# Kernel optimization log

Hardware: AMD Instinct MI355X
Metric: run time of the kernel (lower is better)

Reference implementation:

```python
import jax, jax.numpy as jnp
import numpy as np

N_NODES = 50000
N_EDGES = 800000
IN_FEATS = 256
N_HIDDEN = 256
N_CLASSES = 47


def _glorot(key, shape):
    fan_in, fan_out = shape
    lim = (6.0 / (fan_in + fan_out)) ** 0.5
    return jax.random.uniform(key, shape, jnp.float32, -lim, lim)


def setup_inputs() -> dict:
    key = jax.random.key(0)
    ks = jax.random.split(key, 12)
    x = jax.random.normal(ks[0], (N_NODES, IN_FEATS), jnp.float32)
    src = jax.random.randint(ks[1], (N_EDGES,), 0, N_NODES, jnp.int64)
    dst = jax.random.randint(ks[2], (N_EDGES,), 0, N_NODES, jnp.int64)
    dims = [(IN_FEATS, N_HIDDEN), (N_HIDDEN, N_HIDDEN), (N_HIDDEN, N_CLASSES)]
    inp = {"x": x, "src": src, "dst": dst}
    for i, (di, do) in enumerate(dims):
        inp[f"Wself{i}"] = _glorot(ks[3 + 3 * i], (di, do))
        inp[f"Wneigh{i}"] = _glorot(ks[4 + 3 * i], (di, do))
        inp[f"b{i}"] = jnp.zeros((do,), jnp.float32)
    return inp


def _sage_layer(h, src, dst, Ws, Wn, b):
    # DGL mean SAGEConv: fc_self(h) + fc_neigh(mean over in-neighbors) + bias
    msum = jax.ops.segment_sum(h[src], dst, num_segments=N_NODES)      # [N, d]
    deg = jax.ops.segment_sum(jnp.ones((src.shape[0],), h.dtype), dst,
                              num_segments=N_NODES)                     # [N]
    hmean = msum / jnp.maximum(deg, 1.0)[:, None]
    return h @ Ws + hmean @ Wn + b


def reference(x, src, dst, Wself0, Wneigh0, b0, Wself1, Wneigh1, b1,
              Wself2, Wneigh2, b2):
    h = _sage_layer(x, src, dst, Wself0, Wneigh0, b0)
    h = jax.nn.selu(h)
    h = _sage_layer(h, src, dst, Wself1, Wneigh1, b1)
    h = jax.nn.selu(h)
    h = _sage_layer(h, src, dst, Wself2, Wneigh2, b2)
    return jax.nn.softmax(h, axis=1)
```

## Files before the change

### kernel.cpp

```cpp
#include <hip/hip_runtime.h>
#include <math.h>

#define FEATS 256
#define KTOT  512
#define MS    264
#define SA    40

typedef __attribute__((ext_vector_type(8))) __bf16 bf16x8;
typedef __attribute__((ext_vector_type(4))) float f32x4;

#define ASYNC16(G, L) __builtin_amdgcn_global_load_lds( \
    (const __attribute__((address_space(1))) unsigned int*)(G), \
    (__attribute__((address_space(3))) unsigned int*)(L), 16, 0, 0)

__device__ __forceinline__ float bf2f(unsigned short u) {
    union { unsigned int i; float f; } v; v.i = ((unsigned int)u) << 16; return v.f;
}
__device__ __forceinline__ unsigned short f2bf(float f) {
    unsigned int u = __float_as_uint(f);
    unsigned int r = (u + 0x7FFFu + ((u >> 16) & 1u)) >> 16;
    return (unsigned short)r;
}
__device__ __forceinline__ unsigned short rdw(const void* W, size_t i, bool f32m) {
    return f32m ? f2bf(((const float*)W)[i]) : ((const unsigned short*)W)[i];
}

__global__ void k_detect(const int* __restrict__ srcRaw, const unsigned short* __restrict__ xr,
                         int nE, int* __restrict__ flag) {
    __shared__ int any, cnt;
    if (threadIdx.x == 0) { any = 0; cnt = 0; }
    __syncthreads();
    int lim = nE < 1024 ? nE : 1024;
    for (int i = threadIdx.x; i < lim; i += 256)
        if (srcRaw[2 * i + 1] != 0) atomicAdd(&any, 1);
    int loc = 0;
    for (int i = threadIdx.x; i < 1024; i += 256) {
        unsigned e = (xr[2 * i] >> 7) & 255u;
        if (e >= 90u && e <= 140u) loc++;
    }
    atomicAdd(&cnt, loc);
    __syncthreads();
    if (threadIdx.x == 0) {
        flag[0] = (any == 0) ? 1 : 0;
        flag[1] = (cnt > 512) ? 1 : 0;
    }
}

__global__ void k_count(const int* __restrict__ dstRaw, int* __restrict__ deg, int nE,
                        int nNodes, const int* __restrict__ flag) {
    int e = blockIdx.x * 256 + threadIdx.x;
    if (e >= nE) return;
    int f = flag[0];
    int d = dstRaw[f ? (2 * e) : e];
    if ((unsigned)d >= (unsigned)nNodes) d = 0;
    atomicAdd(&deg[d], 1);
}

__global__ __launch_bounds__(256) void k_bsum(const int* __restrict__ deg, int* __restrict__ bsum,
                                              int n) {
    __shared__ int buf[256];
    const int t = threadIdx.x;
    int i = blockIdx.x * 256 + t;
    buf[t] = (i < n) ? deg[i] : 0;
    __syncthreads();
    for (int s = 128; s > 0; s >>= 1) {
        if (t < s) buf[t] += buf[t + s];
        __syncthreads();
    }
    if (t == 0) bsum[blockIdx.x] = buf[0];
}

__global__ __launch_bounds__(256) void k_scanb(int* __restrict__ bsum, int nB) {
    __shared__ int buf[256];
    __shared__ int carry;
    const int t = threadIdx.x;
    if (t == 0) carry = 0;
    __syncthreads();
    for (int base = 0; base < nB; base += 256) {
        int i = base + t;
        int v = (i < nB) ? bsum[i] : 0;
        buf[t] = v;
        __syncthreads();
        for (int s = 1; s < 256; s <<= 1) {
            int tv = (t >= s) ? buf[t - s] : 0;
            __syncthreads();
            buf[t] += tv;
            __syncthreads();
        }
        int exc = buf[t] - v;
        int c = carry;
        if (i < nB) bsum[i] = c + exc;
        int tot = buf[255];
        __syncthreads();
        if (t == 0) carry = c + tot;
        __syncthreads();
    }
}

__global__ __launch_bounds__(256) void k_offs(const int* __restrict__ deg,
                                              const int* __restrict__ bsum,
                                              int* __restrict__ off, int* __restrict__ cursor,
                                              int n) {
    __shared__ int buf[256];
    const int t = threadIdx.x, b = blockIdx.x;
    int i = b * 256 + t;
    int v = (i < n) ? deg[i] : 0;
    buf[t] = v;
// ... 22 lines not shown
    int pos = atomicAdd(&cursor[d], 1);
    csr[pos] = s;
}

__global__ __launch_bounds__(256) void k_buildAll(
        const void* __restrict__ Ws0, const void* __restrict__ Wn0,
        const void* __restrict__ Ws1, const void* __restrict__ Wn1,
        const void* __restrict__ Ws2, const void* __restrict__ Wn2,
        unsigned short* __restrict__ Wt0, unsigned short* __restrict__ Wt1,
        unsigned short* __restrict__ Wt2s, unsigned short* __restrict__ Wt2n,
        int C, const int* __restrict__ flag) {
    const bool f32m = (flag[1] == 0);
    int idx = blockIdx.x * 256 + threadIdx.x;
    if (idx < 262144) {
        const bool one = idx >= 131072;
        int j = one ? idx - 131072 : idx;
        int n = j >> 9, k = j & 511;
        const void* Ws = one ? Ws1 : Ws0;
        const void* Wn = one ? Wn1 : Wn0;
        unsigned short v = (k < 256) ? rdw(Ws, (size_t)k * 256 + n, f32m)
                                     : rdw(Wn, (size_t)(k - 256) * 256 + n, f32m);
        (one ? Wt1 : Wt0)[j] = v;
    } else if (idx < 294912) {
        const bool nw = idx >= 278528;
        int j = nw ? idx - 278528 : idx - 262144;
        int n = j >> 8, k = j & 255;
        unsigned short v = 0;
        if (n < C) v = rdw(nw ? Wn2 : Ws2, (size_t)k * C + n, f32m);
        (nw ? Wt2n : Wt2s)[j] = v;
    }
}

__global__ __launch_bounds__(256) void k_aggr(
        const void* __restrict__ h, const int* __restrict__ off,
        const int* __restrict__ csr, unsigned short* __restrict__ hmean,
        int M, const int* __restrict__ flag, int maybeF32) {
    const bool f32m = maybeF32 && (flag[1] == 0);
    const int lane = threadIdx.x & 63;
    const int wid = (blockIdx.x * 256 + threadIdx.x) >> 6;
    const int nw = (gridDim.x * 256) >> 6;
    if (f32m) {
        for (int r = wid; r < M; r += nw) {
            const int e0 = off[r], e1 = off[r + 1];
            float a0 = 0.f, a1 = 0.f, a2 = 0.f, a3 = 0.f;
            for (int base = e0; base < e1; base += 64) {
                int cnt = e1 - base; if (cnt > 64) cnt = 64;
                int sidx = (lane < cnt) ? csr[base + lane] : 0;
                #pragma unroll 8
                for (int d = 0; d < cnt; d++) {
                    int s = __shfl(sidx, d);
                    float4 hv = reinterpret_cast<const float4*>(
                        (const float*)h + (size_t)s * FEATS)[lane];
                    a0 += hv.x; a1 += hv.y; a2 += hv.z; a3 += hv.w;
                }
            }
            float rc = 1.0f / fmaxf((float)(e1 - e0), 1.0f);
            ushort4 o;
            o.x = f2bf(a0 * rc); o.y = f2bf(a1 * rc); o.z = f2bf(a2 * rc); o.w = f2bf(a3 * rc);
            *reinterpret_cast<ushort4*>(&hmean[(size_t)r * FEATS + lane * 4]) = o;
        }
    } else {
        for (int r = wid; r < M; r += nw) {
            const int e0 = off[r], e1 = off[r + 1];
            float a0 = 0.f, a1 = 0.f, a2 = 0.f, a3 = 0.f;
            for (int base = e0; base < e1; base += 64) {
                int cnt = e1 - base; if (cnt > 64) cnt = 64;
                int sidx = (lane < cnt) ? csr[base + lane] : 0;
                #pragma unroll 8
                for (int d = 0; d < cnt; d++) {
                    int s = __shfl(sidx, d);
                    ushort4 hv = reinterpret_cast<const ushort4*>(
                        (const unsigned short*)h + (size_t)s * FEATS)[lane];
                    a0 += bf2f(hv.x); a1 += bf2f(hv.y); a2 += bf2f(hv.z); a3 += bf2f(hv.w);
                }
            }
            float rc = 1.0f / fmaxf((float)(e1 - e0), 1.0f);
            ushort4 o;
            o.x = f2bf(a0 * rc); o.y = f2bf(a1 * rc); o.z = f2bf(a2 * rc); o.w = f2bf(a3 * rc);
            *reinterpret_cast<ushort4*>(&hmean[(size_t)r * FEATS + lane * 4]) = o;
        }
    }
}

__global__ __launch_bounds__(256) void k_aggrP(
        const unsigned short* __restrict__ P, const int* __restrict__ off,
        const int* __restrict__ csr, unsigned short* __restrict__ A, int M) {
    const int lane = threadIdx.x & 63;
    const int wid = (blockIdx.x * 256 + threadIdx.x) >> 6;
    const int nw = (gridDim.x * 256) >> 6;
    const int g = lane >> 5, li = lane & 31;
    for (int r = wid; r < M; r += nw) {
        const int e0 = off[r], e1 = off[r + 1];
        float a0 = 0.f, a1 = 0.f;
        #pragma unroll 4
        for (int base = e0; base < e1; base += 2) {
            int e = base + g;
            if (e < e1) {
                int s = csr[e];
                ushort2 hv = *reinterpret_cast<const ushort2*>(
                    P + (size_t)s * 64 + li * 2);
                a0 += bf2f(hv.x); a1 += bf2f(hv.y);
            }
        }
        a0 += __shfl_xor(a0, 32); a1 += __shfl_xor(a1, 32);
        if (g == 0) {
            float rc = 1.0f / fmaxf((float)(e1 - e0), 1.0f);
            unsigned int packed = (unsigned int)f2bf(a0 * rc) |
                                  ((unsigned int)f2bf(a1 * rc) << 16);
            *reinterpret_cast<unsigned int*>(&A[(size_t)r * 64 + li * 2]) = packed;
        }
    }
}

__global__ __launch_bounds__(256) void k_gemm(
        const void* __restrict__ h, const unsigned short* __restrict__ hmean,
        const unsigned short* __restrict__ Wt, const void* __restrict__ bias,
        void* __restrict__ out, int M, const int* __restrict__ flag, int maybeF32) {
    const bool inF32 = (flag[1] == 0);
    const bool hF32 = maybeF32 && inF32;
    __shared__ __align__(16) unsigned short As[64 * 64];
    __shared__ __align__(16) unsigned short Bs[128 * 64];

    const int rb = (int)blockIdx.x >> 1;
    const int chalf = (int)blockIdx.x & 1;
    const int m0 = rb * 64;
    const int col0 = chalf * 128;
    const int tid = threadIdx.x;
    const int lane = tid & 63, w = tid >> 6;
    const int nh = lane & 15, q = lane >> 4;

    f32x4 acc[8];
    #pragma unroll
    for (int ci = 0; ci < 8; ci++) acc[ci] = (f32x4){0.f, 0.f, 0.f, 0.f};

    for (int kb = 0; kb < KTOT; kb += 64) {
        #pragma unroll
        for (int j = 0; j < 2; j++) {
            int t2 = tid + j * 256;
            int row = t2 >> 3, c = t2 & 7;
            int gr = m0 + row; if (gr > M - 1) gr = M - 1;
            int cs = c ^ (row & 7);
            if (kb < 256) {
                if (hF32) {
                    const float* p = (const float*)h + (size_t)gr * FEATS + kb + cs * 8;
                    float4 a = *reinterpret_cast<const float4*>(p);
                    float4 b = *reinterpret_cast<const float4*>(p + 4);
                    unsigned short* d = &As[t2 * 8];
                    d[0]=f2bf(a.x); d[1]=f2bf(a.y); d[2]=f2bf(a.z); d[3]=f2bf(a.w);
                    d[4]=f2bf(b.x); d[5]=f2bf(b.y); d[6]=f2bf(b.z); d[7]=f2bf(b.w);
                } else {
                    ASYNC16((const unsigned short*)h + (size_t)gr * FEATS + kb + cs * 8,
                            &As[t2 * 8]);
                }
            } else {
                ASYNC16(hmean + (size_t)gr * FEATS + (kb - 256) + cs * 8, &As[t2 * 8]);
            }
        }
        #pragma unroll
        for (int j = 0; j < 4; j++) {
            int t2 = tid + j * 256;
            int n = t2 >> 3, c = t2 & 7;
            int cs = c ^ (n & 7);
            ASYNC16(Wt + (size_t)(col0 + n) * KTOT + kb + cs * 8, &Bs[t2 * 8]);
        }
        __syncthreads();

        #pragma unroll
        for (int s = 0; s < 2; s++) {
            const int arow = w * 16 + nh;
            const int qa = ((s * 4 + q) ^ (arow & 7));
            bf16x8 afr = *reinterpret_cast<const bf16x8*>(&As[arow * 64 + qa * 8]);
            #pragma unroll
            for (int ci = 0; ci < 8; ci++) {
                int n = ci * 16 + nh;
                int qb = ((s * 4 + q) ^ (n & 7));
                bf16x8 bfr = *reinterpret_cast<const bf16x8*>(&Bs[n * 64 + qb * 8]);
                acc[ci] = __builtin_amdgcn_mfma_f32_16x16x32_bf16(afr, bfr, acc[ci], 0, 0, 0);
            }
        }
        __syncthreads();
    }

    const int rbase = m0 + w * 16 + q * 4;
    const float sc = 1.0507009873554805f, al = 1.6732632423543772f;
    #pragma unroll
    for (int ci = 0; ci < 8; ci++) {
        int col = col0 + ci * 16 + nh;
        float b = inF32 ? ((const float*)bias)[col] : bf2f(((const unsigned short*)bias)[col]);
        #pragma unroll
        for (int rg = 0; rg < 4; rg++) {
            int r = rbase + rg;
            if (r < M) {
                float v = acc[ci][rg] + b;
                v = (v > 0.f) ? sc * v : sc * al * expm1f(v);
                ((unsigned short*)out)[(size_t)r * FEATS + col] = f2bf(v);
            }
        }
    }
}

__global__ __launch_bounds__(256) void k_gemm256d(
        const unsigned short* __restrict__ h, const unsigned short* __restrict__ Wt2s,
        const unsigned short* __restrict__ Wt2n, float* __restrict__ S2,
        unsigned short* __restrict__ P2, int M) {
    __shared__ __align__(16) unsigned short As[64 * SA];
    __shared__ __align__(16) unsigned short Bs[128 * SA];

    const int m0 = blockIdx.x * 64;
    const int tid = threadIdx.x;
    const int lane = tid & 63, w = tid >> 6;
    const int nh = lane & 15, q = lane >> 4;

    f32x4 acc[8];
    #pragma unroll
    for (int ci = 0; ci < 8; ci++) acc[ci] = (f32x4){0.f, 0.f, 0.f, 0.f};

    for (int kb = 0; kb < 256; kb += 32) {
        {
            int row = tid >> 2, seg = tid & 3;
            int gr = m0 + row; if (gr > M - 1) gr = M - 1;
            *reinterpret_cast<float4*>(&As[row * SA + seg * 8]) =
                *reinterpret_cast<const float4*>(h + (size_t)gr * FEATS + kb + seg * 8);
        }
        for (int u = tid; u < 128 * 4; u += 256) {
            int nn = u >> 2, seg = u & 3;
            const unsigned short* src = (nn < 64)
                ? Wt2s + (size_t)nn * 256 : Wt2n + (size_t)(nn - 64) * 256;
            *reinterpret_cast<float4*>(&Bs[nn * SA + seg * 8]) =
                *reinterpret_cast<const float4*>(src + kb + seg * 8);
        }
        __syncthreads();
        bf16x8 afr = *reinterpret_cast<const bf16x8*>(&As[(w * 16 + nh) * SA + q * 8]);
        #pragma unroll
        for (int ci = 0; ci < 8; ci++) {
            bf16x8 bfr = *reinterpret_cast<const bf16x8*>(&Bs[(ci * 16 + nh) * SA + q * 8]);
            acc[ci] = __builtin_amdgcn_mfma_f32_16x16x32_bf16(afr, bfr, acc[ci], 0, 0, 0);
        }
        __syncthreads();
    }

    const int rbase = m0 + w * 16 + q * 4;
    #pragma unroll
    for (int ci = 0; ci < 4; ci++) {
        int col = ci * 16 + nh;
        #pragma unroll
        for (int rg = 0; rg < 4; rg++) {
            int r = rbase + rg;
            if (r < M) S2[(size_t)r * 64 + col] = acc[ci][rg];
        }
    }
    #pragma unroll
    for (int ci = 4; ci < 8; ci++) {
        int col = (ci - 4) * 16 + nh;
        #pragma unroll
        for (int rg = 0; rg < 4; rg++) {
            int r = rbase + rg;
            if (r < M) P2[(size_t)r * 64 + col] = f2bf(acc[ci][rg]);
        }
    }
}

__global__ __launch_bounds__(256) void k_smax(
        const float* __restrict__ S2, const unsigned short* __restrict__ A2,
        const void* __restrict__ bias, void* __restrict__ out,
        int M, int C, const int* __restrict__ flag) {
    const bool inF32 = (flag[1] == 0);
    const int lane = threadIdx.x & 63;
    const int r = blockIdx.x * 4 + (threadIdx.x >> 6);
    if (r >= M) return;
    float v = -1e30f;
    if (lane < C) {
        float b = inF32 ? ((const float*)bias)[lane]
                        : bf2f(((const unsigned short*)bias)[lane]);
        v = S2[(size_t)r * 64 + lane] + bf2f(A2[(size_t)r * 64 + lane]) + b;
    }
    float mx = v;
    #pragma unroll
    for (int mk = 1; mk <= 32; mk <<= 1) mx = fmaxf(mx, __shfl_xor(mx, mk));
    float e = (lane < C) ? __expf(v - mx) : 0.f;
    float s = e;
    #pragma unroll
    for (int mk = 1; mk <= 32; mk <<= 1) s += __shfl_xor(s, mk);
    float o = e / s;
    if (lane < C) {
        if (inF32) ((float*)out)[(size_t)r * C + lane] = o;
        else ((unsigned short*)out)[(size_t)r * C + lane] = f2bf(o);
    }
}

template <bool F32>
__global__ void k_buildWt(const void* __restrict__ Ws, const void* __restrict__ Wn,
                          unsigned short* __restrict__ Wt, int N, int Npad,
                          const int* __restrict__ flag) {
    if (flag[1] != (F32 ? 0 : 1)) return;
    int idx = blockIdx.x * 256 + threadIdx.x;
    if (idx >= Npad * KTOT) return;
    int n = idx >> 9, k = idx & 511;
    unsigned short v = 0;
    if (n < N) {
        if (F32) {
            float fv = (k < 256) ? ((const float*)Ws)[k * N + n]
                                 : ((const float*)Wn)[(k - 256) * N + n];
            v = f2bf(fv);
        } else {
            v = (k < 256) ? ((const unsigned short*)Ws)[k * N + n]
                          : ((const unsigned short*)Wn)[(k - 256) * N + n];
        }
    }
    Wt[idx] = v;
}

template <bool F32>
__device__ __forceinline__ void stage8(const void* h, size_t elemOff, unsigned short* dst) {
    if (!F32) {
        *reinterpret_cast<float4*>(dst) =
            *reinterpret_cast<const float4*>((const unsigned short*)h + elemOff);
    } else {
        const float* p = (const float*)h + elemOff;
        float4 a = *reinterpret_cast<const float4*>(p);
        float4 b = *reinterpret_cast<const float4*>(p + 4);
        dst[0] = f2bf(a.x); dst[1] = f2bf(a.y); dst[2] = f2bf(a.z); dst[3] = f2bf(a.w);
        dst[4] = f2bf(b.x); dst[5] = f2bf(b.y); dst[6] = f2bf(b.z); dst[7] = f2bf(b.w);
    }
}

template <int NT, int ACT, bool HF32, bool BF32, bool OF32>
__global__ __launch_bounds__(256) void k_sage(
        const void* __restrict__ h, const int* __restrict__ off,
        const int* __restrict__ csr, const unsigned short* __restrict__ Wt,
        const void* __restrict__ bias, void* __restrict__ out,
        int M, int C, const int* __restrict__ flag, int want) {
    if (flag[1] != want) return;
    __shared__ __align__(16) unsigned short meanS[64 * MS];
    __shared__ __align__(16) unsigned short As[64 * SA];
    __shared__ __align__(16) unsigned short Bs[NT * 16 * SA];

    const int m0 = blockIdx.x * 64;
    const int tid = threadIdx.x;
    const int lane = tid & 63, w = tid >> 6;
    const int nh = lane & 15, q = lane >> 4;

    for (int i = 0; i < 16; i++) {
        int lr = w * 16 + i;
        int r = m0 + lr;
        int rr = (r < M) ? r : (M - 1);
        int e0 = off[rr], e1 = off[rr + 1];
        float a0 = 0.f, a1 = 0.f, a2 = 0.f, a3 = 0.f;
        #pragma unroll 8
        for (int j = e0; j < e1; j++) {
            int s = csr[j];
            if (HF32) {
                float4 hv = reinterpret_cast<const float4*>((const float*)h + (size_t)s * FEATS)[lane];
                a0 += hv.x; a1 += hv.y; a2 += hv.z; a3 += hv.w;
            } else {
                ushort4 hv = reinterpret_cast<const ushort4*>((const unsigned short*)h + (size_t)s * FEATS)[lane];
                a0 += bf2f(hv.x); a1 += bf2f(hv.y); a2 += bf2f(hv.z); a3 += bf2f(hv.w);
            }
        }
        float rc = 1.0f / fmaxf((float)(e1 - e0), 1.0f);
        ushort4 o;
        o.x = f2bf(a0 * rc); o.y = f2bf(a1 * rc); o.z = f2bf(a2 * rc); o.w = f2bf(a3 * rc);
        *reinterpret_cast<ushort4*>(&meanS[lr * MS + lane * 4]) = o;
    }
    __syncthreads();

    f32x4 acc[NT];
    #pragma unroll
    for (int ci = 0; ci < NT; ci++) acc[ci] = (f32x4){0.f, 0.f, 0.f, 0.f};

// ... 6 lines not shown
        }
        for (int u = tid; u < NT * 64; u += 256) {
            int nn = u >> 2, seg = u & 3;
            *reinterpret_cast<float4*>(&Bs[nn * SA + seg * 8]) =
                *reinterpret_cast<const float4*>(Wt + (size_t)nn * KTOT + kb + seg * 8);
        }
        __syncthreads();
        bf16x8 afr;
        if (!fromMean)
            afr = *reinterpret_cast<const bf16x8*>(&As[(w * 16 + nh) * SA + q * 8]);
        else
            afr = *reinterpret_cast<const bf16x8*>(&meanS[(w * 16 + nh) * MS + (kb - 256) + q * 8]);
        #pragma unroll
        for (int ci = 0; ci < NT; ci++) {
            bf16x8 bfr = *reinterpret_cast<const bf16x8*>(&Bs[(ci * 16 + nh) * SA + q * 8]);
            acc[ci] = __builtin_amdgcn_mfma_f32_16x16x32_bf16(afr, bfr, acc[ci], 0, 0, 0);
        }
        __syncthreads();
    }

    const int rbase = m0 + w * 16 + q * 4;
    if (ACT == 0) {
        const float sc = 1.0507009873554805f, al = 1.6732632423543772f;
        #pragma unroll
        for (int ci = 0; ci < NT; ci++) {
            int col = ci * 16 + nh;
            float b = BF32 ? ((const float*)bias)[col] : bf2f(((const unsigned short*)bias)[col]);
            #pragma unroll
            for (int rg = 0; rg < 4; rg++) {
                int r = rbase + rg;
                if (r < M) {
                    float v = acc[ci][rg] + b;
                    v = (v > 0.f) ? sc * v : sc * al * expm1f(v);
                    if (OF32) ((float*)out)[(size_t)r * (NT * 16) + col] = v;
                    else ((unsigned short*)out)[(size_t)r * (NT * 16) + col] = f2bf(v);
                }
            }
        }
    } else {
        #pragma unroll
        for (int rg = 0; rg < 4; rg++) {
            int r = rbase + rg;
            float vals[NT];
            float mx = -1e30f;
            #pragma unroll
            for (int ci = 0; ci < NT; ci++) {
                int col = ci * 16 + nh;
                float v = -1e30f;
                if (col < C) {
                    float b = BF32 ? ((const float*)bias)[col] : bf2f(((const unsigned short*)bias)[col]);
                    v = acc[ci][rg] + b;
                }
                vals[ci] = v;
                mx = fmaxf(mx, v);
            }
            #pragma unroll
            for (int mk = 1; mk <= 8; mk <<= 1) mx = fmaxf(mx, __shfl_xor(mx, mk));
            float s = 0.f;
            #pragma unroll
            for (int ci = 0; ci < NT; ci++) {
                float e = (vals[ci] <= -1e29f) ? 0.f : __expf(vals[ci] - mx);
                vals[ci] = e; s += e;
            }
            #pragma unroll
            for (int mk = 1; mk <= 8; mk <<= 1) s += __shfl_xor(s, mk);
            float inv = 1.f / s;
            if (r < M) {
                #pragma unroll
                for (int ci = 0; ci < NT; ci++) {
                    int col = ci * 16 + nh;
                    if (col < C) {
                        if (OF32) ((float*)out)[(size_t)r * C + col] = vals[ci] * inv;
                        else ((unsigned short*)out)[(size_t)r * C + col] = f2bf(vals[ci] * inv);
                    }
                }
            }
        }
    }
}

extern "C" void kernel_launch(void* const* d_in, const int* in_sizes, int n_in,
                              void* d_out, int out_size, void* d_ws, size_t ws_size,
                              hipStream_t stream) {
    const void* x     = d_in[0];
    const int* srcRaw = (const int*)d_in[1];
    const int* dstRaw = (const int*)d_in[2];
    const void* Ws0 = d_in[3]; const void* Wn0 = d_in[4]; const void* b0 = d_in[5];
    const void* Ws1 = d_in[6]; const void* Wn1 = d_in[7]; const void* b1 = d_in[8];
    const void* Ws2 = d_in[9]; const void* Wn2 = d_in[10]; const void* b2 = d_in[11];

    const int nNodes = in_sizes[0] / FEATS;
    const int nE     = in_sizes[1];
    const int C      = in_sizes[11];

    char* ws = (char*)d_ws;
    size_t off_b = 0;
    auto carve = [&](size_t bytes) -> void* {
        void* p = (void*)(ws + off_b);
        off_b += (bytes + 255) & ~(size_t)255;
        return p;
    };
    int*            flag   = (int*)           carve(256);
    int*            deg    = (int*)           carve((size_t)nNodes * 4);
    int*            cursor = (int*)           carve((size_t)nNodes * 4);
    int*            off    = (int*)           carve((size_t)(nNodes + 1) * 4);
    int*            csr    = (int*)           carve((size_t)nE * 4);
    unsigned short* Wt0    = (unsigned short*)carve((size_t)256 * KTOT * 2);
    unsigned short* Wt1    = (unsigned short*)carve((size_t)256 * KTOT * 2);
    unsigned short* Wt2    = (unsigned short*)carve((size_t)64 * KTOT * 2);
    unsigned short* Wt2s   = (unsigned short*)carve((size_t)64 * 256 * 2);
    unsigned short* Wt2n   = (unsigned short*)carve((size_t)64 * 256 * 2);
    int*            bsum   = (int*)           carve(4096);
    unsigned short* hA     = (unsigned short*)carve((size_t)nNodes * FEATS * 2);
    unsigned short* hmean  = (unsigned short*)carve((size_t)nNodes * FEATS * 2);
    const bool split = (off_b <= ws_size);
    const size_t l2n = (size_t)nNodes * 64;
    float*          S2 = (float*)hmean;
    unsigned short* P2 = hmean + l2n * 2;
    unsigned short* A2 = hmean + l2n * 3;
    unsigned short* hX = (unsigned short*)d_in[0];

    const int edgeBlocks = (nE + 255) / 256;
    const int nodeBlocks = (nNodes + 255) / 256;
    const int sageBlocks = (nNodes + 63) / 64;
    const int gemmBlocks = sageBlocks * 2;
    const int aggrBlocks = 2048;
    const int smaxBlocks = (nNodes + 3) / 4;

    k_detect<<<1, 256, 0, stream>>>(srcRaw, (const unsigned short*)x, nE, flag);
    hipMemsetAsync(deg, 0, (size_t)nNodes * 4, stream);
    k_count<<<edgeBlocks, 256, 0, stream>>>(dstRaw, deg, nE, nNodes, flag);
    k_bsum<<<nodeBlocks, 256, 0, stream>>>(deg, bsum, nNodes);
    k_scanb<<<1, 256, 0, stream>>>(bsum, nodeBlocks);
    k_offs<<<nodeBlocks, 256, 0, stream>>>(deg, bsum, off, cursor, nNodes);
    k_fill<<<edgeBlocks, 256, 0, stream>>>(srcRaw, dstRaw, cursor, csr, nE, nNodes, flag);

    if (split) {
        k_buildAll<<<(294912 + 255) / 256, 256, 0, stream>>>(
            Ws0, Wn0, Ws1, Wn1, Ws2, Wn2, Wt0, Wt1, Wt2s, Wt2n, C, flag);

        k_aggr<<<aggrBlocks, 256, 0, stream>>>(x, off, csr, hmean, nNodes, flag, 1);
        k_gemm<<<gemmBlocks, 256, 0, stream>>>(x, hmean, Wt0, b0, hA, nNodes, flag, 1);

        k_aggr<<<aggrBlocks, 256, 0, stream>>>(hA, off, csr, hmean, nNodes, flag, 0);
        k_gemm<<<gemmBlocks, 256, 0, stream>>>(hA, hmean, Wt1, b1, hX, nNodes, flag, 0);

        k_gemm256d<<<sageBlocks, 256, 0, stream>>>(hX, Wt2s, Wt2n, S2, P2, nNodes);
        k_aggrP<<<aggrBlocks, 256, 0, stream>>>(P2, off, csr, A2, nNodes);
        k_smax<<<smaxBlocks, 256, 0, stream>>>(S2, A2, b2, d_out, nNodes, C, flag);
    } else {
        int wtB = (256 * KTOT + 255) / 256;
        k_buildWt<false><<<wtB, 256, 0, stream>>>(Ws0, Wn0, Wt0, 256, 256, flag);
        k_buildWt<true ><<<wtB, 256, 0, stream>>>(Ws0, Wn0, Wt0, 256, 256, flag);
        k_buildWt<false><<<wtB, 256, 0, stream>>>(Ws1, Wn1, Wt1, 256, 256, flag);
        k_buildWt<true ><<<wtB, 256, 0, stream>>>(Ws1, Wn1, Wt1, 256, 256, flag);
        int wtB2 = (64 * KTOT + 255) / 256;
        k_buildWt<false><<<wtB2, 256, 0, stream>>>(Ws2, Wn2, Wt2, C, 64, flag);
        k_buildWt<true ><<<wtB2, 256, 0, stream>>>(Ws2, Wn2, Wt2, C, 64, flag);
        k_sage<16, 0, false, false, false><<<sageBlocks, 256, 0, stream>>>(
            x, off, csr, Wt0, b0, hA, nNodes, 256, flag, 1);
        k_sage<16, 0, true, true, false><<<sageBlocks, 256, 0, stream>>>(
            x, off, csr, Wt0, b0, hA, nNodes, 256, flag, 0);
        k_sage<16, 0, false, false, false><<<sageBlocks, 256, 0, stream>>>(
            hA, off, csr, Wt1, b1, hX, nNodes, 256, flag, 1);
        k_sage<16, 0, false, true, false><<<sageBlocks, 256, 0, stream>>>(
            hA, off, csr, Wt1, b1, hX, nNodes, 256, flag, 0);
        k_sage<4, 1, false, false, false><<<sageBlocks, 256, 0, stream>>>(
            hX, off, csr, Wt2, b2, d_out, nNodes, C, flag, 1);
        k_sage<4, 1, false, true, true><<<sageBlocks, 256, 0, stream>>>(
            hX, off, csr, Wt2, b2, d_out, nNodes, C, flag, 0);
    }
}
```

Measured before the change: 541.9 us.

## Fuse graph preprocessing into one cooperative kernel and merge final aggregation with softmax

Replaces the chain of preprocessing kernels (detect, memset, degree count, block sums, scan, offsets, CSR fill, weight transpose) with a single cooperative kernel that uses grid-wide syncs between phases. It falls back to the old launch sequence if the cooperative launch fails. It also fuses the last-layer neighbor aggregation with bias add and softmax, so the intermediate A2 buffer is never written and read back. The aim is to cut launch overhead and one global round trip. The cost is grid.sync barriers and a fixed grid of 1024 blocks for the atomic-heavy phases.

```diff
diff --git a/kernel.cpp b/kernel.cpp
--- a/kernel.cpp
+++ b/kernel.cpp
@@ -1,5 +1,8 @@
 #include <hip/hip_runtime.h>
+#include <hip/hip_cooperative_groups.h>
 #include <math.h>
+
+namespace cg = cooperative_groups;
 
 #define FEATS 256
 #define KTOT  512
@@ -23,6 +26,131 @@
 }
 __device__ __forceinline__ unsigned short rdw(const void* W, size_t i, bool f32m) {
     return f32m ? f2bf(((const float*)W)[i]) : ((const unsigned short*)W)[i];
+}
+
+__global__ __launch_bounds__(256) void k_prep(
+        const int* srcRaw, const int* dstRaw, const unsigned short* xr,
+        int nE, int nNodes, int nodeBlocks, int C,
+        int* flag, int* deg, int* bsum, int* off, int* cursor, int* csr,
+        const void* Ws0, const void* Wn0, const void* Ws1, const void* Wn1,
+        const void* Ws2, const void* Wn2,
+        unsigned short* Wt0, unsigned short* Wt1,
+        unsigned short* Wt2s, unsigned short* Wt2n) {
+    cg::grid_group grid = cg::this_grid();
+    const int tid = threadIdx.x;
+    const int gid = blockIdx.x * 256 + tid;
+    const int gsz = gridDim.x * 256;
+    __shared__ int buf[256];
+    __shared__ int sAny, sCnt, carry;
+
+    for (int i = gid; i < nNodes; i += gsz) deg[i] = 0;
+    if (blockIdx.x == 0) {
+        if (tid == 0) { sAny = 0; sCnt = 0; }
+        __syncthreads();
+        int lim = nE < 1024 ? nE : 1024;
+        for (int i = tid; i < lim; i += 256)
+            if (srcRaw[2 * i + 1] != 0) atomicAdd(&sAny, 1);
+        int loc = 0;
+        for (int i = tid; i < 1024; i += 256) {
+            unsigned e = (xr[2 * i] >> 7) & 255u;
+            if (e >= 90u && e <= 140u) loc++;
+        }
+        atomicAdd(&sCnt, loc);
+        __syncthreads();
+        if (tid == 0) { flag[0] = (sAny == 0) ? 1 : 0; flag[1] = (sCnt > 512) ? 1 : 0; }
+    }
+    grid.sync();
+
+    const int f = flag[0];
+    const bool f32m = (flag[1] == 0);
+    for (int e = gid; e < nE; e += gsz) {
+        int d = dstRaw[f ? (2 * e) : e];
+        if ((unsigned)d >= (unsigned)nNodes) d = 0;
+        atomicAdd(&deg[d], 1);
+    }
+    for (int idx = gid; idx < 294912; idx += gsz) {
+        if (idx < 262144) {
+            const bool one = idx >= 131072;
+            int j = one ? idx - 131072 : idx;
+            int n = j >> 9, k = j & 511;
+            const void* Ws = one ? Ws1 : Ws0;
+            const void* Wn = one ? Wn1 : Wn0;
+            unsigned short v = (k < 256) ? rdw(Ws, (size_t)k * 256 + n, f32m)
+                                         : rdw(Wn, (size_t)(k - 256) * 256 + n, f32m);
+            (one ? Wt1 : Wt0)[j] = v;
+        } else {
+            const bool nw = idx >= 278528;
+            int j = nw ? idx - 278528 : idx - 262144;
+            int n = j >> 8, k = j & 255;
+            unsigned short v = 0;
+            if (n < C) v = rdw(nw ? Wn2 : Ws2, (size_t)k * C + n, f32m);
+            (nw ? Wt2n : Wt2s)[j] = v;
+        }
+    }
+    grid.sync();
+
+    if (blockIdx.x < nodeBlocks) {
+        int i = blockIdx.x * 256 + tid;
+        buf[tid] = (i < nNodes) ? deg[i] : 0;
+        __syncthreads();
+        for (int s = 128; s > 0; s >>= 1) {
+            if (tid < s) buf[tid] += buf[tid + s];
+            __syncthreads();
+        }
+        if (tid == 0) bsum[blockIdx.x] = buf[0];
+    }
+    grid.sync();
+
+    if (blockIdx.x == 0) {
+        if (tid == 0) carry = 0;
+        __syncthreads();
+        for (int base = 0; base < nodeBlocks; base += 256) {
+            int i = base + tid;
+            int v = (i < nodeBlocks) ? bsum[i] : 0;
+            buf[tid] = v;
+            __syncthreads();
+            for (int s = 1; s < 256; s <<= 1) {
+                int tv = (tid >= s) ? buf[tid - s] : 0;
+                __syncthreads();
+                buf[tid] += tv;
+                __syncthreads();
+            }
+            int exc = buf[tid] - v;
+            int c = carry;
+            if (i < nodeBlocks) bsum[i] = c + exc;
+            int tot = buf[255];
+            __syncthreads();
+            if (tid == 0) carry = c + tot;
+            __syncthreads();
+        }
+    }
+    grid.sync();
+
+    if (blockIdx.x < nodeBlocks) {
+        int i = blockIdx.x * 256 + tid;
+        int v = (i < nNodes) ? deg[i] : 0;
+        buf[tid] = v;
+        __syncthreads();
+        for (int s = 1; s < 256; s <<= 1) {
+            int tv = (tid >= s) ? buf[tid - s] : 0;
+            __syncthreads();
+            buf[tid] += tv;
+            __syncthreads();
+        }
+        int exc = bsum[blockIdx.x] + buf[tid] - v;
+        if (i < nNodes) { off[i] = exc; cursor[i] = exc; }
+        if (i == nNodes - 1) off[nNodes] = exc + v;
+    }
+    grid.sync();
+
+    for (int e = gid; e < nE; e += gsz) {
+        int d = dstRaw[f ? (2 * e) : e];
+        int s = srcRaw[f ? (2 * e) : e];
+        if ((unsigned)d >= (unsigned)nNodes) d = 0;
+        if ((unsigned)s >= (unsigned)nNodes) s = 0;
+        int pos = atomicAdd(&cursor[d], 1);
+        csr[pos] = s;
+    }
 }
 
 __global__ void k_detect(const int* __restrict__ srcRaw, const unsigned short* __restrict__ xr,
@@ -211,36 +339,6 @@
     }
 }
 
-__global__ __launch_bounds__(256) void k_aggrP(
-        const unsigned short* __restrict__ P, const int* __restrict__ off,
-        const int* __restrict__ csr, unsigned short* __restrict__ A, int M) {
-    const int lane = threadIdx.x & 63;
-    const int wid = (blockIdx.x * 256 + threadIdx.x) >> 6;
-    const int nw = (gridDim.x * 256) >> 6;
-    const int g = lane >> 5, li = lane & 31;
-    for (int r = wid; r < M; r += nw) {
-        const int e0 = off[r], e1 = off[r + 1];
-        float a0 = 0.f, a1 = 0.f;
-        #pragma unroll 4
-        for (int base = e0; base < e1; base += 2) {
-            int e = base + g;
-            if (e < e1) {
-                int s = csr[e];
-                ushort2 hv = *reinterpret_cast<const ushort2*>(
-                    P + (size_t)s * 64 + li * 2);
-                a0 += bf2f(hv.x); a1 += bf2f(hv.y);
-            }
-        }
-        a0 += __shfl_xor(a0, 32); a1 += __shfl_xor(a1, 32);
-        if (g == 0) {
-            float rc = 1.0f / fmaxf((float)(e1 - e0), 1.0f);
-            unsigned int packed = (unsigned int)f2bf(a0 * rc) |
-                                  ((unsigned int)f2bf(a1 * rc) << 16);
-            *reinterpret_cast<unsigned int*>(&A[(size_t)r * 64 + li * 2]) = packed;
-        }
-    }
-}
-
 __global__ __launch_bounds__(256) void k_gemm(
         const void* __restrict__ h, const unsigned short* __restrict__ hmean,
         const unsigned short* __restrict__ Wt, const void* __restrict__ bias,
@@ -389,31 +487,52 @@
     }
 }
 
-__global__ __launch_bounds__(256) void k_smax(
-        const float* __restrict__ S2, const unsigned short* __restrict__ A2,
+__global__ __launch_bounds__(256) void k_aggrsm(
+        const unsigned short* __restrict__ P, const float* __restrict__ S2,
+        const int* __restrict__ off, const int* __restrict__ csr,
         const void* __restrict__ bias, void* __restrict__ out,
         int M, int C, const int* __restrict__ flag) {
     const bool inF32 = (flag[1] == 0);
     const int lane = threadIdx.x & 63;
-    const int r = blockIdx.x * 4 + (threadIdx.x >> 6);
-    if (r >= M) return;
-    float v = -1e30f;
-    if (lane < C) {
-        float b = inF32 ? ((const float*)bias)[lane]
-                        : bf2f(((const unsigned short*)bias)[lane]);
-        v = S2[(size_t)r * 64 + lane] + bf2f(A2[(size_t)r * 64 + lane]) + b;
-    }
-    float mx = v;
-    #pragma unroll
-    for (int mk = 1; mk <= 32; mk <<= 1) mx = fmaxf(mx, __shfl_xor(mx, mk));
-    float e = (lane < C) ? __expf(v - mx) : 0.f;
-    float s = e;
-    #pragma unroll
-    for (int mk = 1; mk <= 32; mk <<= 1) s += __shfl_xor(s, mk);
-    float o = e / s;
-    if (lane < C) {
-        if (inF32) ((float*)out)[(size_t)r * C + lane] = o;
-        else ((unsigned short*)out)[(size_t)r * C + lane] = f2bf(o);
+    const int wid = (blockIdx.x * 256 + threadIdx.x) >> 6;
+    const int nw = (gridDim.x * 256) >> 6;
+    const int g = lane >> 5, li = lane & 31;
+    for (int r = wid; r < M; r += nw) {
+        const int e0 = off[r], e1 = off[r + 1];
+        float a0 = 0.f, a1 = 0.f;
+        #pragma unroll 4
+        for (int base = e0; base < e1; base += 2) {
+            int e = base + g;
+            if (e < e1) {
+                int s = csr[e];
+                ushort2 hv = *reinterpret_cast<const ushort2*>(
+                    P + (size_t)s * 64 + li * 2);
+                a0 += bf2f(hv.x); a1 += bf2f(hv.y);
+            }
+        }
+        a0 += __shfl_xor(a0, 32); a1 += __shfl_xor(a1, 32);
+        float rc = 1.0f / fmaxf((float)(e1 - e0), 1.0f);
+        float av0 = __shfl(a0, lane >> 1);
+        float av1 = __shfl(a1, lane >> 1);
+        float av = (lane & 1) ? av1 : av0;
+        float v = -1e30f;
+        if (lane < C) {
+            float b = inF32 ? ((const float*)bias)[lane]
+                            : bf2f(((const unsigned short*)bias)[lane]);
+            v = S2[(size_t)r * 64 + lane] + av * rc + b;
+        }
+        float mx = v;
+        #pragma unroll
+        for (int mk = 1; mk <= 32; mk <<= 1) mx = fmaxf(mx, __shfl_xor(mx, mk));
+        float e = (lane < C) ? __expf(v - mx) : 0.f;
+        float s = e;
+        #pragma unroll
+        for (int mk = 1; mk <= 32; mk <<= 1) s += __shfl_xor(s, mk);
+        float o = e / s;
+        if (lane < C) {
+            if (inF32) ((float*)out)[(size_t)r * C + lane] = o;
+            else ((unsigned short*)out)[(size_t)r * C + lane] = f2bf(o);
+        }
     }
 }
 
@@ -586,9 +705,9 @@
 extern "C" void kernel_launch(void* const* d_in, const int* in_sizes, int n_in,
                               void* d_out, int out_size, void* d_ws, size_t ws_size,
                               hipStream_t stream) {
-    const void* x     = d_in[0];
     const int* srcRaw = (const int*)d_in[1];
     const int* dstRaw = (const int*)d_in[2];
+    const void* x   = d_in[0];
     const void* Ws0 = d_in[3]; const void* Wn0 = d_in[4]; const void* b0 = d_in[5];
     const void* Ws1 = d_in[6]; const void* Wn1 = d_in[7]; const void* b1 = d_in[8];
     const void* Ws2 = d_in[9]; const void* Wn2 = d_in[10]; const void* b2 = d_in[11];
@@ -621,7 +740,6 @@
     const size_t l2n = (size_t)nNodes * 64;
     float*          S2 = (float*)hmean;
     unsigned short* P2 = hmean + l2n * 2;
-    unsigned short* A2 = hmean + l2n * 3;
     unsigned short* hX = (unsigned short*)d_in[0];
 
     const int edgeBlocks = (nE + 255) / 256;
@@ -629,19 +747,32 @@
     const int sageBlocks = (nNodes + 63) / 64;
     const int gemmBlocks = sageBlocks * 2;
     const int aggrBlocks = 2048;
-    const int smaxBlocks = (nNodes + 3) / 4;
-
-    k_detect<<<1, 256, 0, stream>>>(srcRaw, (const unsigned short*)x, nE, flag);
-    hipMemsetAsync(deg, 0, (size_t)nNodes * 4, stream);
-    k_count<<<edgeBlocks, 256, 0, stream>>>(dstRaw, deg, nE, nNodes, flag);
-    k_bsum<<<nodeBlocks, 256, 0, stream>>>(deg, bsum, nNodes);
-    k_scanb<<<1, 256, 0, stream>>>(bsum, nodeBlocks);
-    k_offs<<<nodeBlocks, 256, 0, stream>>>(deg, bsum, off, cursor, nNodes);
-    k_fill<<<edgeBlocks, 256, 0, stream>>>(srcRaw, dstRaw, cursor, csr, nE, nNodes, flag);
 
     if (split) {
-        k_buildAll<<<(294912 + 255) / 256, 256, 0, stream>>>(
-            Ws0, Wn0, Ws1, Wn1, Ws2, Wn2, Wt0, Wt1, Wt2s, Wt2n, C, flag);
+        const unsigned short* xr = (const unsigned short*)x;
+        int nE_v = nE, nN_v = nNodes, nB_v = nodeBlocks, C_v = C;
+        void* cargs[] = {
+            (void*)&srcRaw, (void*)&dstRaw, (void*)&xr,
+            (void*)&nE_v, (void*)&nN_v, (void*)&nB_v, (void*)&C_v,
+            (void*)&flag, (void*)&deg, (void*)&bsum, (void*)&off,
+            (void*)&cursor, (void*)&csr,
+            (void*)&Ws0, (void*)&Wn0, (void*)&Ws1, (void*)&Wn1,
+            (void*)&Ws2, (void*)&Wn2,
+            (void*)&Wt0, (void*)&Wt1, (void*)&Wt2s, (void*)&Wt2n };
+        hipError_t ce = hipLaunchCooperativeKernel(k_prep, dim3(1024), dim3(256),
+                                                   cargs, 0, stream);
+        if (ce != hipSuccess) {
+            k_detect<<<1, 256, 0, stream>>>(srcRaw, xr, nE, flag);
+            hipError_t me = hipMemsetAsync(deg, 0, (size_t)nNodes * 4, stream);
+            (void)me;
+            k_count<<<edgeBlocks, 256, 0, stream>>>(dstRaw, deg, nE, nNodes, flag);
+            k_bsum<<<nodeBlocks, 256, 0, stream>>>(deg, bsum, nNodes);
+            k_scanb<<<1, 256, 0, stream>>>(bsum, nodeBlocks);
+            k_offs<<<nodeBlocks, 256, 0, stream>>>(deg, bsum, off, cursor, nNodes);
+            k_fill<<<edgeBlocks, 256, 0, stream>>>(srcRaw, dstRaw, cursor, csr, nE, nNodes, flag);
+            k_buildAll<<<(294912 + 255) / 256, 256, 0, stream>>>(
+                Ws0, Wn0, Ws1, Wn1, Ws2, Wn2, Wt0, Wt1, Wt2s, Wt2n, C, flag);
+        }
 
         k_aggr<<<aggrBlocks, 256, 0, stream>>>(x, off, csr, hmean, nNodes, flag, 1);
         k_gemm<<<gemmBlocks, 256, 0, stream>>>(x, hmean, Wt0, b0, hA, nNodes, flag, 1);
@@ -650,9 +781,18 @@
         k_gemm<<<gemmBlocks, 256, 0, stream>>>(hA, hmean, Wt1, b1, hX, nNodes, flag, 0);
 
         k_gemm256d<<<sageBlocks, 256, 0, stream>>>(hX, Wt2s, Wt2n, S2, P2, nNodes);
-        k_aggrP<<<aggrBlocks, 256, 0, stream>>>(P2, off, csr, A2, nNodes);
-        k_smax<<<smaxBlocks, 256, 0, stream>>>(S2, A2, b2, d_out, nNodes, C, flag);
+        k_aggrsm<<<aggrBlocks, 256, 0, stream>>>(P2, S2, off, csr, b2, d_out,
+                                                 nNodes, C, flag);
     } else {
+        const unsigned short* xr = (const unsigned short*)x;
+        k_detect<<<1, 256, 0, stream>>>(srcRaw, xr, nE, flag);
+        hipError_t me = hipMemsetAsync(deg, 0, (size_t)nNodes * 4, stream);
+        (void)me;
+        k_count<<<edgeBlocks, 256, 0, stream>>>(dstRaw, deg, nE, nNodes, flag);
+        k_bsum<<<nodeBlocks, 256, 0, stream>>>(deg, bsum, nNodes);
+        k_scanb<<<1, 256, 0, stream>>>(bsum, nodeBlocks);
+        k_offs<<<nodeBlocks, 256, 0, stream>>>(deg, bsum, off, cursor, nNodes);
+        k_fill<<<edgeBlocks, 256, 0, stream>>>(srcRaw, dstRaw, cursor, csr, nE, nNodes, flag);
         int wtB = (256 * KTOT + 255) / 256;
         k_buildWt<false><<<wtB, 256, 0, stream>>>(Ws0, Wn0, Wt0, 256, 256, flag);
         k_buildWt<true ><<<wtB, 256, 0, stream>>>(Ws0, Wn0, Wt0, 256, 256, flag);
```

Result: slower. 1.091 ms (+101.3%).

## Double-buffer GEMM LDS tiles and fuse final aggregation with softmax

Applied to the files above, without the earlier changes.

Adds double buffering to the main SAGE GEMM so the next K-tile is staged into a second LDS buffer while MFMAs run on the current one, with one barrier per iteration. The last layer's neighbor aggregation and softmax are merged into one kernel, removing the intermediate aggregated buffer and one launch. Doubled LDS per block may lower occupancy, and the single-barrier scheme relies on async LDS loads being waited at the barrier.

```diff
diff --git a/kernel.cpp b/kernel.cpp
--- a/kernel.cpp
+++ b/kernel.cpp
@@ -211,9 +211,166 @@
     }
 }
 
-__global__ __launch_bounds__(256) void k_aggrP(
-        const unsigned short* __restrict__ P, const int* __restrict__ off,
-        const int* __restrict__ csr, unsigned short* __restrict__ A, int M) {
+__global__ __launch_bounds__(256) void k_gemm(
+        const void* __restrict__ h, const unsigned short* __restrict__ hmean,
+        const unsigned short* __restrict__ Wt, const void* __restrict__ bias,
+        void* __restrict__ out, int M, const int* __restrict__ flag, int maybeF32) {
+    const bool inF32 = (flag[1] == 0);
+    const bool hF32 = maybeF32 && inF32;
+    __shared__ __align__(16) unsigned short As[2][64 * 64];
+    __shared__ __align__(16) unsigned short Bs[2][128 * 64];
+
+    const int rb = (int)blockIdx.x >> 1;
+    const int chalf = (int)blockIdx.x & 1;
+    const int m0 = rb * 64;
+    const int col0 = chalf * 128;
+    const int tid = threadIdx.x;
+    const int lane = tid & 63, w = tid >> 6;
+    const int nh = lane & 15, q = lane >> 4;
+
+    f32x4 acc[8];
+    #pragma unroll
+    for (int ci = 0; ci < 8; ci++) acc[ci] = (f32x4){0.f, 0.f, 0.f, 0.f};
+
+    auto stageAB = [&](int bsel, int kb) {
+        #pragma unroll
+        for (int j = 0; j < 2; j++) {
+            int t2 = tid + j * 256;
+            int row = t2 >> 3, c = t2 & 7;
+            int gr = m0 + row; if (gr > M - 1) gr = M - 1;
+            int cs = c ^ (row & 7);
+            if (kb < 256) {
+                if (hF32) {
+                    const float* p = (const float*)h + (size_t)gr * FEATS + kb + cs * 8;
+                    float4 a = *reinterpret_cast<const float4*>(p);
+                    float4 b = *reinterpret_cast<const float4*>(p + 4);
+                    unsigned short* d = &As[bsel][t2 * 8];
+                    d[0]=f2bf(a.x); d[1]=f2bf(a.y); d[2]=f2bf(a.z); d[3]=f2bf(a.w);
+                    d[4]=f2bf(b.x); d[5]=f2bf(b.y); d[6]=f2bf(b.z); d[7]=f2bf(b.w);
+                } else {
+                    ASYNC16((const unsigned short*)h + (size_t)gr * FEATS + kb + cs * 8,
+                            &As[bsel][t2 * 8]);
+                }
+            } else {
+                ASYNC16(hmean + (size_t)gr * FEATS + (kb - 256) + cs * 8, &As[bsel][t2 * 8]);
+            }
+        }
+        #pragma unroll
+        for (int j = 0; j < 4; j++) {
+            int t2 = tid + j * 256;
+            int n = t2 >> 3, c = t2 & 7;
+            int cs = c ^ (n & 7);
+            ASYNC16(Wt + (size_t)(col0 + n) * KTOT + kb + cs * 8, &Bs[bsel][t2 * 8]);
+        }
+    };
+
+    stageAB(0, 0);
+    __syncthreads();
+    int cur = 0;
+    for (int kb = 0; kb < KTOT; kb += 64) {
+        if (kb + 64 < KTOT) stageAB(cur ^ 1, kb + 64);
+        #pragma unroll
+        for (int s = 0; s < 2; s++) {
+            const int arow = w * 16 + nh;
+            const int qa = ((s * 4 + q) ^ (arow & 7));
+            bf16x8 afr = *reinterpret_cast<const bf16x8*>(&As[cur][arow * 64 + qa * 8]);
+            #pragma unroll
+            for (int ci = 0; ci < 8; ci++) {
+                int n = ci * 16 + nh;
+                int qb = ((s * 4 + q) ^ (n & 7));
+                bf16x8 bfr = *reinterpret_cast<const bf16x8*>(&Bs[cur][n * 64 + qb * 8]);
+                acc[ci] = __builtin_amdgcn_mfma_f32_16x16x32_bf16(afr, bfr, acc[ci], 0, 0, 0);
+            }
+        }
+        __syncthreads();
+        cur ^= 1;
+    }
+
+    const int rbase = m0 + w * 16 + q * 4;
+    const float sc = 1.0507009873554805f, al = 1.6732632423543772f;
+    #pragma unroll
+    for (int ci = 0; ci < 8; ci++) {
+        int col = col0 + ci * 16 + nh;
+        float b = inF32 ? ((const float*)bias)[col] : bf2f(((const unsigned short*)bias)[col]);
+        #pragma unroll
+        for (int rg = 0; rg < 4; rg++) {
+            int r = rbase + rg;
+            if (r < M) {
+                float v = acc[ci][rg] + b;
+                v = (v > 0.f) ? sc * v : sc * al * expm1f(v);
+                ((unsigned short*)out)[(size_t)r * FEATS + col] = f2bf(v);
+            }
+        }
+    }
+}
+
+__global__ __launch_bounds__(256) void k_gemm256d(
+        const unsigned short* __restrict__ h, const unsigned short* __restrict__ Wt2s,
+        const unsigned short* __restrict__ Wt2n, float* __restrict__ S2,
+        unsigned short* __restrict__ P2, int M) {
+    __shared__ __align__(16) unsigned short As[64 * SA];
+    __shared__ __align__(16) unsigned short Bs[128 * SA];
+
+    const int m0 = blockIdx.x * 64;
+    const int tid = threadIdx.x;
+    const int lane = tid & 63, w = tid >> 6;
+    const int nh = lane & 15, q = lane >> 4;
+
+    f32x4 acc[8];
+    #pragma unroll
+    for (int ci = 0; ci < 8; ci++) acc[ci] = (f32x4){0.f, 0.f, 0.f, 0.f};
+
+    for (int kb = 0; kb < 256; kb += 32) {
+        {
+            int row = tid >> 2, seg = tid & 3;
+            int gr = m0 + row; if (gr > M - 1) gr = M - 1;
+            *reinterpret_cast<float4*>(&As[row * SA + seg * 8]) =
+                *reinterpret_cast<const float4*>(h + (size_t)gr * FEATS + kb + seg * 8);
+        }
+        for (int u = tid; u < 128 * 4; u += 256) {
+            int nn = u >> 2, seg = u & 3;
+            const unsigned short* src = (nn < 64)
+                ? Wt2s + (size_t)nn * 256 : Wt2n + (size_t)(nn - 64) * 256;
+            *reinterpret_cast<float4*>(&Bs[nn * SA + seg * 8]) =
+                *reinterpret_cast<const float4*>(src + kb + seg * 8);
+        }
+        __syncthreads();
+        bf16x8 afr = *reinterpret_cast<const bf16x8*>(&As[(w * 16 + nh) * SA + q * 8]);
+        #pragma unroll
+        for (int ci = 0; ci < 8; ci++) {
+            bf16x8 bfr = *reinterpret_cast<const bf16x8*>(&Bs[(ci * 16 + nh) * SA + q * 8]);
+            acc[ci] = __builtin_amdgcn_mfma_f32_16x16x32_bf16(afr, bfr, acc[ci], 0, 0, 0);
+        }
+        __syncthreads();
+    }
+
+    const int rbase = m0 + w * 16 + q * 4;
+    #pragma unroll
+    for (int ci = 0; ci < 4; ci++) {
+        int col = ci * 16 + nh;
+        #pragma unroll
+        for (int rg = 0; rg < 4; rg++) {
+            int r = rbase + rg;
+            if (r < M) S2[(size_t)r * 64 + col] = acc[ci][rg];
+        }
+    }
+    #pragma unroll
+    for (int ci = 4; ci < 8; ci++) {
+        int col = (ci - 4) * 16 + nh;
+        #pragma unroll
+        for (int rg = 0; rg < 4; rg++) {
+            int r = rbase + rg;
+            if (r < M) P2[(size_t)r * 64 + col] = f2bf(acc[ci][rg]);
+        }
+    }
+}
+
+__global__ __launch_bounds__(256) void k_aggrsm(
+        const unsigned short* __restrict__ P, const float* __restrict__ S2,
+        const int* __restrict__ off, const int* __restrict__ csr,
+        const void* __restrict__ bias, void* __restrict__ out,
+        int M, int C, const int* __restrict__ flag) {
+    const bool inF32 = (flag[1] == 0);
     const int lane = threadIdx.x & 63;
     const int wid = (blockIdx.x * 256 + threadIdx.x) >> 6;
     const int nw = (gridDim.x * 256) >> 6;
@@ -232,188 +389,28 @@
             }
         }
         a0 += __shfl_xor(a0, 32); a1 += __shfl_xor(a1, 32);
-        if (g == 0) {
-            float rc = 1.0f / fmaxf((float)(e1 - e0), 1.0f);
-            unsigned int packed = (unsigned int)f2bf(a0 * rc) |
-                                  ((unsigned int)f2bf(a1 * rc) << 16);
-            *reinterpret_cast<unsigned int*>(&A[(size_t)r * 64 + li * 2]) = packed;
-        }
-    }
-}
-
-__global__ __launch_bounds__(256) void k_gemm(
-        const void* __restrict__ h, const unsigned short* __restrict__ hmean,
-        const unsigned short* __restrict__ Wt, const void* __restrict__ bias,
-        void* __restrict__ out, int M, const int* __restrict__ flag, int maybeF32) {
-    const bool inF32 = (flag[1] == 0);
-    const bool hF32 = maybeF32 && inF32;
-    __shared__ __align__(16) unsigned short As[64 * 64];
-    __shared__ __align__(16) unsigned short Bs[128 * 64];
-
-    const int rb = (int)blockIdx.x >> 1;
-    const int chalf = (int)blockIdx.x & 1;
-    const int m0 = rb * 64;
-    const int col0 = chalf * 128;
-    const int tid = threadIdx.x;
-    const int lane = tid & 63, w = tid >> 6;
-    const int nh = lane & 15, q = lane >> 4;
-
-    f32x4 acc[8];
-    #pragma unroll
-    for (int ci = 0; ci < 8; ci++) acc[ci] = (f32x4){0.f, 0.f, 0.f, 0.f};
-
-    for (int kb = 0; kb < KTOT; kb += 64) {
-        #pragma unroll
-        for (int j = 0; j < 2; j++) {
-            int t2 = tid + j * 256;
-            int row = t2 >> 3, c = t2 & 7;
-            int gr = m0 + row; if (gr > M - 1) gr = M - 1;
-            int cs = c ^ (row & 7);
-            if (kb < 256) {
-                if (hF32) {
-                    const float* p = (const float*)h + (size_t)gr * FEATS + kb + cs * 8;
-                    float4 a = *reinterpret_cast<const float4*>(p);
-                    float4 b = *reinterpret_cast<const float4*>(p + 4);
-                    unsigned short* d = &As[t2 * 8];
-                    d[0]=f2bf(a.x); d[1]=f2bf(a.y); d[2]=f2bf(a.z); d[3]=f2bf(a.w);
-                    d[4]=f2bf(b.x); d[5]=f2bf(b.y); d[6]=f2bf(b.z); d[7]=f2bf(b.w);
-                } else {
-                    ASYNC16((const unsigned short*)h + (size_t)gr * FEATS + kb + cs * 8,
-                            &As[t2 * 8]);
-                }
-            } else {
-                ASYNC16(hmean + (size_t)gr * FEATS + (kb - 256) + cs * 8, &As[t2 * 8]);
-            }
-        }
-        #pragma unroll
-        for (int j = 0; j < 4; j++) {
-            int t2 = tid + j * 256;
-            int n = t2 >> 3, c = t2 & 7;
-            int cs = c ^ (n & 7);
-            ASYNC16(Wt + (size_t)(col0 + n) * KTOT + kb + cs * 8, &Bs[t2 * 8]);
-        }
-        __syncthreads();
-
-        #pragma unroll
-        for (int s = 0; s < 2; s++) {
-            const int arow = w * 16 + nh;
-            const int qa = ((s * 4 + q) ^ (arow & 7));
-            bf16x8 afr = *reinterpret_cast<const bf16x8*>(&As[arow * 64 + qa * 8]);
-            #pragma unroll
-            for (int ci = 0; ci < 8; ci++) {
-                int n = ci * 16 + nh;
-                int qb = ((s * 4 + q) ^ (n & 7));
-                bf16x8 bfr = *reinterpret_cast<const bf16x8*>(&Bs[n * 64 + qb * 8]);
-                acc[ci] = __builtin_amdgcn_mfma_f32_16x16x32_bf16(afr, bfr, acc[ci], 0, 0, 0);
-            }
-        }
-        __syncthreads();
-    }
-
-    const int rbase = m0 + w * 16 + q * 4;
-    const float sc = 1.0507009873554805f, al = 1.6732632423543772f;
-    #pragma unroll
-    for (int ci = 0; ci < 8; ci++) {
-        int col = col0 + ci * 16 + nh;
-        float b = inF32 ? ((const float*)bias)[col] : bf2f(((const unsigned short*)bias)[col]);
-        #pragma unroll
-        for (int rg = 0; rg < 4; rg++) {
-            int r = rbase + rg;
-            if (r < M) {
-                float v = acc[ci][rg] + b;
-                v = (v > 0.f) ? sc * v : sc * al * expm1f(v);
-                ((unsigned short*)out)[(size_t)r * FEATS + col] = f2bf(v);
-            }
-        }
-    }
-}
-
-__global__ __launch_bounds__(256) void k_gemm256d(
-        const unsigned short* __restrict__ h, const unsigned short* __restrict__ Wt2s,
-        const unsigned short* __restrict__ Wt2n, float* __restrict__ S2,
-        unsigned short* __restrict__ P2, int M) {
-    __shared__ __align__(16) unsigned short As[64 * SA];
-    __shared__ __align__(16) unsigned short Bs[128 * SA];
-
-    const int m0 = blockIdx.x * 64;
-    const int tid = threadIdx.x;
-    const int lane = tid & 63, w = tid >> 6;
-    const int nh = lane & 15, q = lane >> 4;
-
-    f32x4 acc[8];
-    #pragma unroll
-    for (int ci = 0; ci < 8; ci++) acc[ci] = (f32x4){0.f, 0.f, 0.f, 0.f};
-
-    for (int kb = 0; kb < 256; kb += 32) {
-        {
-            int row = tid >> 2, seg = tid & 3;
-            int gr = m0 + row; if (gr > M - 1) gr = M - 1;
-            *reinterpret_cast<float4*>(&As[row * SA + seg * 8]) =
-                *reinterpret_cast<const float4*>(h + (size_t)gr * FEATS + kb + seg * 8);
-        }
-        for (int u = tid; u < 128 * 4; u += 256) {
-            int nn = u >> 2, seg = u & 3;
-            const unsigned short* src = (nn < 64)
-                ? Wt2s + (size_t)nn * 256 : Wt2n + (size_t)(nn - 64) * 256;
-            *reinterpret_cast<float4*>(&Bs[nn * SA + seg * 8]) =
-                *reinterpret_cast<const float4*>(src + kb + seg * 8);
-        }
-        __syncthreads();
-        bf16x8 afr = *reinterpret_cast<const bf16x8*>(&As[(w * 16 + nh) * SA + q * 8]);
-        #pragma unroll
-        for (int ci = 0; ci < 8; ci++) {
-            bf16x8 bfr = *reinterpret_cast<const bf16x8*>(&Bs[(ci * 16 + nh) * SA + q * 8]);
-            acc[ci] = __builtin_amdgcn_mfma_f32_16x16x32_bf16(afr, bfr, acc[ci], 0, 0, 0);
-        }
-        __syncthreads();
-    }
-
-    const int rbase = m0 + w * 16 + q * 4;
-    #pragma unroll
-    for (int ci = 0; ci < 4; ci++) {
-        int col = ci * 16 + nh;
-        #pragma unroll
-        for (int rg = 0; rg < 4; rg++) {
-            int r = rbase + rg;
-            if (r < M) S2[(size_t)r * 64 + col] = acc[ci][rg];
-        }
-    }
-    #pragma unroll
-    for (int ci = 4; ci < 8; ci++) {
-        int col = (ci - 4) * 16 + nh;
-        #pragma unroll
-        for (int rg = 0; rg < 4; rg++) {
-            int r = rbase + rg;
-            if (r < M) P2[(size_t)r * 64 + col] = f2bf(acc[ci][rg]);
-        }
-    }
-}
-
-__global__ __launch_bounds__(256) void k_smax(
-        const float* __restrict__ S2, const unsigned short* __restrict__ A2,
-        const void* __restrict__ bias, void* __restrict__ out,
-        int M, int C, const int* __restrict__ flag) {
-    const bool inF32 = (flag[1] == 0);
-    const int lane = threadIdx.x & 63;
-    const int r = blockIdx.x * 4 + (threadIdx.x >> 6);
-    if (r >= M) return;
-    float v = -1e30f;
-    if (lane < C) {
-        float b = inF32 ? ((const float*)bias)[lane]
-                        : bf2f(((const unsigned short*)bias)[lane]);
-        v = S2[(size_t)r * 64 + lane] + bf2f(A2[(size_t)r * 64 + lane]) + b;
-    }
-    float mx = v;
-    #pragma unroll
-    for (int mk = 1; mk <= 32; mk <<= 1) mx = fmaxf(mx, __shfl_xor(mx, mk));
-    float e = (lane < C) ? __expf(v - mx) : 0.f;
-    float s = e;
-    #pragma unroll
-    for (int mk = 1; mk <= 32; mk <<= 1) s += __shfl_xor(s, mk);
-    float o = e / s;
-    if (lane < C) {
-        if (inF32) ((float*)out)[(size_t)r * C + lane] = o;
-        else ((unsigned short*)out)[(size_t)r * C + lane] = f2bf(o);
+        float rc = 1.0f / fmaxf((float)(e1 - e0), 1.0f);
+        float av0 = __shfl(a0, lane >> 1);
+        float av1 = __shfl(a1, lane >> 1);
+        float av = (lane & 1) ? av1 : av0;
+        float v = -1e30f;
+        if (lane < C) {
+            float b = inF32 ? ((const float*)bias)[lane]
+                            : bf2f(((const unsigned short*)bias)[lane]);
+            v = S2[(size_t)r * 64 + lane] + av * rc + b;
+        }
+        float mx = v;
+        #pragma unroll
+        for (int mk = 1; mk <= 32; mk <<= 1) mx = fmaxf(mx, __shfl_xor(mx, mk));
+        float e = (lane < C) ? __expf(v - mx) : 0.f;
+        float s = e;
+        #pragma unroll
+        for (int mk = 1; mk <= 32; mk <<= 1) s += __shfl_xor(s, mk);
+        float o = e / s;
+        if (lane < C) {
+            if (inF32) ((float*)out)[(size_t)r * C + lane] = o;
+            else ((unsigned short*)out)[(size_t)r * C + lane] = f2bf(o);
+        }
     }
 }
 
@@ -586,9 +583,9 @@
 extern "C" void kernel_launch(void* const* d_in, const int* in_sizes, int n_in,
                               void* d_out, int out_size, void* d_ws, size_t ws_size,
                               hipStream_t stream) {
-    const void* x     = d_in[0];
     const int* srcRaw = (const int*)d_in[1];
     const int* dstRaw = (const int*)d_in[2];
+    const void* x   = d_in[0];
     const void* Ws0 = d_in[3]; const void* Wn0 = d_in[4]; const void* b0 = d_in[5];
     const void* Ws1 = d_in[6]; const void* Wn1 = d_in[7]; const void* b1 = d_in[8];
     const void* Ws2 = d_in[9]; const void* Wn2 = d_in[10]; const void* b2 = d_in[11];
@@ -621,7 +618,6 @@
     const size_t l2n = (size_t)nNodes * 64;
     float*          S2 = (float*)hmean;
     unsigned short* P2 = hmean + l2n * 2;
-    unsigned short* A2 = hmean + l2n * 3;
     unsigned short* hX = (unsigned short*)d_in[0];
 
     const int edgeBlocks = (nE + 255) / 256;
@@ -629,10 +625,11 @@
     const int sageBlocks = (nNodes + 63) / 64;
     const int gemmBlocks = sageBlocks * 2;
     const int aggrBlocks = 2048;
-    const int smaxBlocks = (nNodes + 3) / 4;
-
-    k_detect<<<1, 256, 0, stream>>>(srcRaw, (const unsigned short*)x, nE, flag);
-    hipMemsetAsync(deg, 0, (size_t)nNodes * 4, stream);
+
+    const unsigned short* xr = (const unsigned short*)x;
+    k_detect<<<1, 256, 0, stream>>>(srcRaw, xr, nE, flag);
+    hipError_t me = hipMemsetAsync(deg, 0, (size_t)nNodes * 4, stream);
+    (void)me;
     k_count<<<edgeBlocks, 256, 0, stream>>>(dstRaw, deg, nE, nNodes, flag);
     k_bsum<<<nodeBlocks, 256, 0, stream>>>(deg, bsum, nNodes);
     k_scanb<<<1, 256, 0, stream>>>(bsum, nodeBlocks);
@@ -650,8 +647,8 @@
         k_gemm<<<gemmBlocks, 256, 0, stream>>>(hA, hmean, Wt1, b1, hX, nNodes, flag, 0);
 
         k_gemm256d<<<sageBlocks, 256, 0, stream>>>(hX, Wt2s, Wt2n, S2, P2, nNodes);
-        k_aggrP<<<aggrBlocks, 256, 0, stream>>>(P2, off, csr, A2, nNodes);
-        k_smax<<<smaxBlocks, 256, 0, stream>>>(S2, A2, b2, d_out, nNodes, C, flag);
+        k_aggrsm<<<aggrBlocks, 256, 0, stream>>>(P2, S2, off, csr, b2, d_out,
+                                                 nNodes, C, flag);
     } else {
         int wtB = (256 * KTOT + 255) / 256;
         k_buildWt<false><<<wtB, 256, 0, stream>>>(Ws0, Wn0, Wt0, 256, 256, flag);
```

Result: slower. 563.8 us (+4.0%).
